# Kernel tuning notes

Hardware: AMD Instinct MI355X
Metric: run time of the kernel (lower is better)

Reference implementation:

```python
import jax, jax.numpy as jnp
import numpy as np

B, D_W, D_C, D_P = 4096, 2048, 1024, 2048
RANK = D_W // 4  # 512, per A_U/A_V shapes (d_w, d_w//4)


def setup_inputs() -> dict:
    key = jax.random.key(0)
    ks = jax.random.split(key, 10)
    return {
        "w_prev": jax.random.normal(ks[0], (B, D_W), jnp.float32),
        "z_t": jax.random.normal(ks[1], (B, D_P), jnp.float32),
        "c_t": jax.random.normal(ks[2], (B, D_C), jnp.float32),
        # params (mirroring flax init: A_diag zeros, A_U/A_V normal(0.01),
        # Dense kernels lecun_normal-ish scale, zero biases)
        "A_diag": jnp.zeros((D_W,), jnp.float32),
        "A_U": 0.01 * jax.random.normal(ks[3], (D_W, RANK), jnp.float32),
        "A_V": 0.01 * jax.random.normal(ks[4], (D_W, RANK), jnp.float32),
        "W_mod": jax.random.normal(ks[5], (D_C, D_W), jnp.float32) / np.sqrt(D_C),
        "b_mod": jnp.zeros((D_W,), jnp.float32),
        "W_B": jax.random.normal(ks[6], (D_C + D_P, D_W), jnp.float32) / np.sqrt(D_C + D_P),
        "b_B": jnp.zeros((D_W,), jnp.float32),
    }


def reference(w_prev, z_t, c_t, A_diag, A_U, A_V, W_mod, b_mod, W_B, b_B):
    # A = diag(tanh(A_diag)*0.9) + A_U @ A_V^T, row-scaled by modulation.
    # Equivalent (same math) without materializing [B, d_w, d_w]:
    #   (A * m[:, :, None]) @ w = m * (a_diag * w + A_U @ (A_V^T @ w))
    a_diag = jnp.tanh(A_diag) * 0.9                              # [d_w]
    modulation = jnp.tanh(c_t @ W_mod + b_mod)                   # [B, d_w]
    Aw = a_diag * w_prev + (w_prev @ A_V) @ A_U.T                # [B, d_w]
    Bt = jnp.concatenate([c_t, z_t], axis=-1) @ W_B + b_B        # [B, d_w]
    return modulation * Aw + Bt
```

## Files before the change

### kernel.cpp

```cpp
#include <hip/hip_runtime.h>


#define DEV __device__ __forceinline__

typedef __bf16 v8bf __attribute__((ext_vector_type(8)));
typedef __bf16 v4bf __attribute__((ext_vector_type(4)));
typedef float  v4f  __attribute__((ext_vector_type(4)));

typedef __attribute__((address_space(1))) const unsigned int* as1_cuint_ptr;
typedef __attribute__((address_space(3))) unsigned int*       as3_uint_ptr;

DEV void async16(const void* g, void* l) {
  __builtin_amdgcn_global_load_lds(
      (as1_cuint_ptr)(unsigned long long)g,
      (as3_uint_ptr)(unsigned long long)l,
      16, 0, 0);
}

DEV float tanh_fast(float x) {
  x = fminf(15.f, fmaxf(-15.f, x));
  float e = __expf(2.f * x);
  return (e - 1.f) / (e + 1.f);
}


__global__ void cvt_all(const float* __restrict__ w, const float* __restrict__ z,
                        const float* __restrict__ c, const float* __restrict__ au,
                        const float* __restrict__ av,
                        __bf16* __restrict__ wb, __bf16* __restrict__ zb,
                        __bf16* __restrict__ cb, __bf16* __restrict__ aub,
                        __bf16* __restrict__ avb) {
  int b = blockIdx.x;
  const float* src; __bf16* dst; int off;
  if (b < 8192)        { src = w;  dst = wb;  off = b; }
  else if (b < 16384)  { src = z;  dst = zb;  off = b - 8192; }
  else if (b < 20480)  { src = c;  dst = cb;  off = b - 16384; }
  else if (b < 21504)  { src = au; dst = aub; off = b - 20480; }
  else                 { src = av; dst = avb; off = b - 21504; }
  size_t i = (size_t)off * 1024 + (size_t)threadIdx.x * 4;
  float4 v = *reinterpret_cast<const float4*>(src + i);
  v4bf o;
  o.x = (__bf16)v.x; o.y = (__bf16)v.y; o.z = (__bf16)v.z; o.w = (__bf16)v.w;
  *reinterpret_cast<v4bf*>(dst + i) = o;
}

__global__ void transpose_both(const float* __restrict__ Wmod,
                               const float* __restrict__ WB,
                               __bf16* __restrict__ Wmodt,
                               __bf16* __restrict__ WBt) {
  __shared__ float t[32][33];
  int b = blockIdx.x;
  const float* src; __bf16* dst; int R;
  if (b < 2048) { src = Wmod; dst = Wmodt; R = 1024; }
  else          { b -= 2048; src = WB; dst = WBt; R = 3072; }
  const int c0 = (b & 63) * 32, r0 = (b >> 6) * 32;
  const int C = 2048;
  const int tx = threadIdx.x & 31, ty = threadIdx.x >> 5;
#pragma unroll
  for (int rr = 0; rr < 32; rr += 8)
    t[ty + rr][tx] = src[(size_t)(r0 + ty + rr) * C + c0 + tx];
  __syncthreads();
#pragma unroll
  for (int rr = 0; rr < 32; rr += 8)
    dst[(size_t)(c0 + ty + rr) * R + r0 + tx] = (__bf16)t[tx][ty + rr];
}

__global__ __launch_bounds__(256, 2) void gemm_mt(
    const __bf16* __restrict__ A0, const __bf16* __restrict__ Bt,
    int N, int K, __bf16* __restrict__ out, const float* __restrict__ A_diag) {
  __shared__ __align__(16) __bf16 As[128 * 32];
  __shared__ __align__(16) __bf16 Bs[128 * 32];

  const int tid = threadIdx.x, lane = tid & 63, wid = tid >> 6;
  const int wm = wid >> 1, wn = wid & 1, l16 = lane & 15, quad = lane >> 4;
  const int m0 = blockIdx.y * 128, n0 = blockIdx.x * 128;
  const int sg_row = lane >> 2;
  const int sk = ((lane & 3) ^ ((lane >> 3) & 3)) * 8;
  const int qs = quad ^ ((l16 >> 1) & 3);

  v4f acc[4][4];
#pragma unroll
  for (int i = 0; i < 4; ++i)
#pragma unroll
    for (int j = 0; j < 4; ++j) { v4f zz = {0,0,0,0}; acc[i][j] = zz; }

  for (int k0 = 0; k0 < K; k0 += 32) {
    __syncthreads();
#pragma unroll
    for (int t = 0; t < 2; ++t) {
      const int chunk = wid * 2 + t;
      const int row = chunk * 16 + sg_row;
      async16((const void*)(A0 + (size_t)(m0 + row) * K + k0 + sk),
              (void*)&As[chunk * 512 + lane * 8]);
      async16((const void*)(Bt + (size_t)(n0 + row) * K + k0 + sk),
              (void*)&Bs[chunk * 512 + lane * 8]);
    }
    __syncthreads();
    const v8bf* Ap = reinterpret_cast<const v8bf*>(As);
    const v8bf* Bp = reinterpret_cast<const v8bf*>(Bs);
    v8bf a[4], b[4];
#pragma unroll
    for (int i = 0; i < 4; ++i) a[i] = Ap[(wm * 64 + i * 16 + l16) * 4 + qs];
#pragma unroll
    for (int j = 0; j < 4; ++j) b[j] = Bp[(wn * 64 + j * 16 + l16) * 4 + qs];
#pragma unroll
    for (int i = 0; i < 4; ++i)
#pragma unroll
      for (int j = 0; j < 4; ++j)
        acc[i][j] = __builtin_amdgcn_mfma_f32_16x16x32_bf16(a[i], b[j],
                                                            acc[i][j], 0, 0, 0);
  }

  const int mBase = m0 + wm * 64 + quad * 4;
  const int nBase = n0 + wn * 64 + l16;
#pragma unroll
  for (int j = 0; j < 4; ++j) {
    const int n = nBase + j * 16;
#pragma unroll
    for (int i = 0; i < 4; ++i)
#pragma unroll
      for (int r = 0; r < 4; ++r) {
        const int m = mBase + i * 16 + r;
        float v = acc[i][j][r];
        if (m == n) v += tanh_fast(A_diag[m]) * 0.9f;
        out[(size_t)m * N + n] = (__bf16)v;
      }
  }
}

__global__ __launch_bounds__(256, 2) void fused_main(
    const __bf16* __restrict__ c, const __bf16* __restrict__ z,
    const __bf16* __restrict__ w, const __bf16* __restrict__ Wmodt,
    const __bf16* __restrict__ Mt, const __bf16* __restrict__ WBt,
    const float* __restrict__ b_mod, const float* __restrict__ b_B,
    float* __restrict__ out) {
  constexpr int DC = 1024, DW = 2048, KB = 3072;
  __shared__ __align__(16) __bf16 As[128 * 32];
  __shared__ __align__(16) __bf16 Bs[128 * 32];

  const int tid = threadIdx.x, lane = tid & 63, wid = tid >> 6;
  const int wm = wid >> 1, wn = wid & 1, l16 = lane & 15, quad = lane >> 4;
  const int m0 = blockIdx.y * 128;
  const int n0 = blockIdx.x * 128;
  const int sg_row = lane >> 2;
  const int sk = ((lane & 3) ^ ((lane >> 3) & 3)) * 8;
  const int qs = quad ^ ((l16 >> 1) & 3);
  const int ldsA  = (wid * 2) * 512 + lane * 8;
  const int ldsA2 = (wid * 2 + 1) * 512 + lane * 8;
  const int rowA  = (wid * 2) * 16 + sg_row;
  const int rowA2 = (wid * 2 + 1) * 16 + sg_row;

  v4f acc[4][4];
#pragma unroll
  for (int i = 0; i < 4; ++i)
#pragma unroll
    for (int j = 0; j < 4; ++j) { v4f zz = {0,0,0,0}; acc[i][j] = zz; }

  auto kstep = [&](const __bf16* gA, size_t lda, const __bf16* gB, size_t ldb,
                   int kA, int kB) {
    __syncthreads();
    async16((const void*)(gA + (size_t)(m0 + rowA) * lda + kA + sk),
            (void*)&As[ldsA]);
    async16((const void*)(gB + (size_t)(n0 + rowA) * ldb + kB + sk),
            (void*)&Bs[ldsA]);
    async16((const void*)(gA + (size_t)(m0 + rowA2) * lda + kA + sk),
            (void*)&As[ldsA2]);
    async16((const void*)(gB + (size_t)(n0 + rowA2) * ldb + kB + sk),
            (void*)&Bs[ldsA2]);
    __syncthreads();
    const v8bf* Ap = reinterpret_cast<const v8bf*>(As);
    const v8bf* Bp = reinterpret_cast<const v8bf*>(Bs);
    v8bf a[4], b[4];
#pragma unroll
    for (int i = 0; i < 4; ++i) a[i] = Ap[(wm * 64 + i * 16 + l16) * 4 + qs];
#pragma unroll
    for (int j = 0; j < 4; ++j) b[j] = Bp[(wn * 64 + j * 16 + l16) * 4 + qs];
#pragma unroll
    for (int i = 0; i < 4; ++i)
#pragma unroll
      for (int j = 0; j < 4; ++j)
        acc[i][j] = __builtin_amdgcn_mfma_f32_16x16x32_bf16(a[i], b[j],
                                                            acc[i][j], 0, 0, 0);
  };

  const int nBase = n0 + wn * 64 + l16;

  for (int k0 = 0; k0 < DC; k0 += 32) kstep(c, DC, Wmodt, DC, k0, k0);

  v4f mod_s[4][4];
#pragma unroll
  for (int j = 0; j < 4; ++j) {
    const float bn = b_mod[nBase + j * 16];
#pragma unroll
    for (int i = 0; i < 4; ++i) {
#pragma unroll
      for (int r = 0; r < 4; ++r)
        mod_s[i][j][r] = tanh_fast(acc[i][j][r] + bn);
      v4f zz = {0,0,0,0};
      acc[i][j] = zz;
    }
  }

  for (int k0 = 0; k0 < DW; k0 += 32) kstep(w, DW, Mt, DW, k0, k0);

#pragma unroll
  for (int i = 0; i < 4; ++i)
#pragma unroll
    for (int j = 0; j < 4; ++j) acc[i][j] *= mod_s[i][j];

  for (int k0 = 0; k0 < DC; k0 += 32) kstep(c, DC, WBt, KB, k0, k0);
  for (int k0 = DC; k0 < KB; k0 += 32) kstep(z, DW, WBt, KB, k0 - DC, k0);

  const int mBase = m0 + wm * 64 + quad * 4;
#pragma unroll
  for (int j = 0; j < 4; ++j) {
    const int n = nBase + j * 16;
    const float bn = b_B[n];
#pragma unroll
    for (int i = 0; i < 4; ++i)
#pragma unroll
      for (int r = 0; r < 4; ++r) {
        const int m = mBase + i * 16 + r;
        out[(size_t)m * DW + n] = acc[i][j][r] + bn;
      }
  }
}


extern "C" void kernel_launch(void* const* d_in, const int* in_sizes, int n_in,
                              void* d_out, int out_size, void* d_ws,
                              size_t ws_size, hipStream_t stream) {
  const float* w_prev = (const float*)d_in[0];
  const float* z_t    = (const float*)d_in[1];
  const float* c_t    = (const float*)d_in[2];
  const float* A_diag = (const float*)d_in[3];
  const float* A_U    = (const float*)d_in[4];
  const float* A_V    = (const float*)d_in[5];
  const float* W_mod  = (const float*)d_in[6];
  const float* b_mod  = (const float*)d_in[7];
  const float* W_B    = (const float*)d_in[8];
  const float* b_B    = (const float*)d_in[9];

  constexpr int Bsz = 4096, DW = 2048, RK = 512;
  const size_t MB = 1ull << 20;
  char* ws = (char*)d_ws;
  __bf16* w_bf  = (__bf16*)(ws + 0);
  __bf16* z_bf  = (__bf16*)(ws + 16 * MB);
  __bf16* c_bf  = (__bf16*)(ws + 32 * MB);
  __bf16* AU_bf = (__bf16*)(ws + 40 * MB);
  __bf16* AV_bf = (__bf16*)(ws + 42 * MB);
  __bf16* Wmodt = (__bf16*)(ws + 44 * MB);
  __bf16* WBt   = (__bf16*)(ws + 48 * MB);
  __bf16* Mt    = (__bf16*)(ws + 60 * MB);

  cvt_all<<<22528, 256, 0, stream>>>(w_prev, z_t, c_t, A_U, A_V,
                                     w_bf, z_bf, c_bf, AU_bf, AV_bf);
  transpose_both<<<2048 + 6144, 256, 0, stream>>>(W_mod, W_B, Wmodt, WBt);

  gemm_mt<<<dim3(DW / 128, DW / 128), 256, 0, stream>>>(AU_bf, AV_bf, DW, RK,
                                                        Mt, A_diag);

  fused_main<<<dim3(DW / 128, Bsz / 128), 256, 0, stream>>>(
      c_bf, z_bf, w_bf, Wmodt, Mt, WBt, b_mod, b_B, (float*)d_out);
}
```

Measured before the change: 314.3 us.

## Shrink fused GEMM tile to 128x64 with higher occupancy; merge prep kernels

The main fused GEMM now uses 128x64 output tiles instead of 128x128, with half the accumulator registers per warp, and raises launch bounds to 4 blocks per CU. This doubles the block count (1024 blocks) for better latency hiding with the single-buffered, synchronous-per-kstep loads. It also merges the conversion and transpose prep kernels into one launch to save a launch gap. The trade-off is lower arithmetic intensity: A tiles get reloaded twice as often, and there are more MFMA-unfriendly syncs per flop.

```diff
diff --git a/kernel.cpp b/kernel.cpp
--- a/kernel.cpp
+++ b/kernel.cpp
@@ -23,33 +23,31 @@
   return (e - 1.f) / (e + 1.f);
 }
 
-
-__global__ void cvt_all(const float* __restrict__ w, const float* __restrict__ z,
-                        const float* __restrict__ c, const float* __restrict__ au,
-                        const float* __restrict__ av,
-                        __bf16* __restrict__ wb, __bf16* __restrict__ zb,
-                        __bf16* __restrict__ cb, __bf16* __restrict__ aub,
-                        __bf16* __restrict__ avb) {
-  int b = blockIdx.x;
-  const float* src; __bf16* dst; int off;
-  if (b < 8192)        { src = w;  dst = wb;  off = b; }
-  else if (b < 16384)  { src = z;  dst = zb;  off = b - 8192; }
-  else if (b < 20480)  { src = c;  dst = cb;  off = b - 16384; }
-  else if (b < 21504)  { src = au; dst = aub; off = b - 20480; }
-  else                 { src = av; dst = avb; off = b - 21504; }
-  size_t i = (size_t)off * 1024 + (size_t)threadIdx.x * 4;
-  float4 v = *reinterpret_cast<const float4*>(src + i);
-  v4bf o;
-  o.x = (__bf16)v.x; o.y = (__bf16)v.y; o.z = (__bf16)v.z; o.w = (__bf16)v.w;
-  *reinterpret_cast<v4bf*>(dst + i) = o;
-}
-
-__global__ void transpose_both(const float* __restrict__ Wmod,
-                               const float* __restrict__ WB,
-                               __bf16* __restrict__ Wmodt,
-                               __bf16* __restrict__ WBt) {
+__global__ void prep(const float* __restrict__ w, const float* __restrict__ z,
+                     const float* __restrict__ c, const float* __restrict__ au,
+                     const float* __restrict__ av,
+                     const float* __restrict__ Wmod, const float* __restrict__ WB,
+                     __bf16* __restrict__ wb, __bf16* __restrict__ zb,
+                     __bf16* __restrict__ cb, __bf16* __restrict__ aub,
+                     __bf16* __restrict__ avb,
+                     __bf16* __restrict__ Wmodt, __bf16* __restrict__ WBt) {
   __shared__ float t[32][33];
   int b = blockIdx.x;
+  if (b < 22528) {
+    const float* src; __bf16* dst; int off;
+    if (b < 8192)        { src = w;  dst = wb;  off = b; }
+    else if (b < 16384)  { src = z;  dst = zb;  off = b - 8192; }
+    else if (b < 20480)  { src = c;  dst = cb;  off = b - 16384; }
+    else if (b < 21504)  { src = au; dst = aub; off = b - 20480; }
+    else                 { src = av; dst = avb; off = b - 21504; }
+    size_t i = (size_t)off * 1024 + (size_t)threadIdx.x * 4;
+    float4 v = *reinterpret_cast<const float4*>(src + i);
+    v4bf o;
+    o.x = (__bf16)v.x; o.y = (__bf16)v.y; o.z = (__bf16)v.z; o.w = (__bf16)v.w;
+    *reinterpret_cast<v4bf*>(dst + i) = o;
+    return;
+  }
+  b -= 22528;
   const float* src; __bf16* dst; int R;
   if (b < 2048) { src = Wmod; dst = Wmodt; R = 1024; }
   else          { b -= 2048; src = WB; dst = WBt; R = 3072; }
@@ -128,7 +126,7 @@
   }
 }
 
-__global__ __launch_bounds__(256, 2) void fused_main(
+__global__ __launch_bounds__(256, 4) void fused_main(
     const __bf16* __restrict__ c, const __bf16* __restrict__ z,
     const __bf16* __restrict__ w, const __bf16* __restrict__ Wmodt,
     const __bf16* __restrict__ Mt, const __bf16* __restrict__ WBt,
@@ -136,60 +134,60 @@
     float* __restrict__ out) {
   constexpr int DC = 1024, DW = 2048, KB = 3072;
   __shared__ __align__(16) __bf16 As[128 * 32];
-  __shared__ __align__(16) __bf16 Bs[128 * 32];
+  __shared__ __align__(16) __bf16 Bs[64 * 32];
 
   const int tid = threadIdx.x, lane = tid & 63, wid = tid >> 6;
   const int wm = wid >> 1, wn = wid & 1, l16 = lane & 15, quad = lane >> 4;
   const int m0 = blockIdx.y * 128;
-  const int n0 = blockIdx.x * 128;
+  const int n0 = blockIdx.x * 64;
   const int sg_row = lane >> 2;
   const int sk = ((lane & 3) ^ ((lane >> 3) & 3)) * 8;
   const int qs = quad ^ ((l16 >> 1) & 3);
-  const int ldsA  = (wid * 2) * 512 + lane * 8;
-  const int ldsA2 = (wid * 2 + 1) * 512 + lane * 8;
-  const int rowA  = (wid * 2) * 16 + sg_row;
-  const int rowA2 = (wid * 2 + 1) * 16 + sg_row;
-
-  v4f acc[4][4];
+  const int rowA0 = wid * 32 + sg_row;
+  const int rowA1 = wid * 32 + 16 + sg_row;
+  const int rowB  = wid * 16 + sg_row;
+  const int ldsA0 = (wid * 2) * 512 + lane * 8;
+  const int ldsA1 = (wid * 2 + 1) * 512 + lane * 8;
+  const int ldsB  = wid * 512 + lane * 8;
+
+  v4f acc[4][2];
 #pragma unroll
   for (int i = 0; i < 4; ++i)
 #pragma unroll
-    for (int j = 0; j < 4; ++j) { v4f zz = {0,0,0,0}; acc[i][j] = zz; }
+    for (int j = 0; j < 2; ++j) { v4f zz = {0,0,0,0}; acc[i][j] = zz; }
 
   auto kstep = [&](const __bf16* gA, size_t lda, const __bf16* gB, size_t ldb,
                    int kA, int kB) {
     __syncthreads();
-    async16((const void*)(gA + (size_t)(m0 + rowA) * lda + kA + sk),
-            (void*)&As[ldsA]);
-    async16((const void*)(gB + (size_t)(n0 + rowA) * ldb + kB + sk),
-            (void*)&Bs[ldsA]);
-    async16((const void*)(gA + (size_t)(m0 + rowA2) * lda + kA + sk),
-            (void*)&As[ldsA2]);
-    async16((const void*)(gB + (size_t)(n0 + rowA2) * ldb + kB + sk),
-            (void*)&Bs[ldsA2]);
+    async16((const void*)(gA + (size_t)(m0 + rowA0) * lda + kA + sk),
+            (void*)&As[ldsA0]);
+    async16((const void*)(gA + (size_t)(m0 + rowA1) * lda + kA + sk),
+            (void*)&As[ldsA1]);
+    async16((const void*)(gB + (size_t)(n0 + rowB) * ldb + kB + sk),
+            (void*)&Bs[ldsB]);
     __syncthreads();
     const v8bf* Ap = reinterpret_cast<const v8bf*>(As);
     const v8bf* Bp = reinterpret_cast<const v8bf*>(Bs);
-    v8bf a[4], b[4];
+    v8bf a[4], b[2];
 #pragma unroll
     for (int i = 0; i < 4; ++i) a[i] = Ap[(wm * 64 + i * 16 + l16) * 4 + qs];
 #pragma unroll
-    for (int j = 0; j < 4; ++j) b[j] = Bp[(wn * 64 + j * 16 + l16) * 4 + qs];
-#pragma unroll
-    for (int i = 0; i < 4; ++i)
-#pragma unroll
-      for (int j = 0; j < 4; ++j)
+    for (int j = 0; j < 2; ++j) b[j] = Bp[(wn * 32 + j * 16 + l16) * 4 + qs];
+#pragma unroll
+    for (int i = 0; i < 4; ++i)
+#pragma unroll
+      for (int j = 0; j < 2; ++j)
         acc[i][j] = __builtin_amdgcn_mfma_f32_16x16x32_bf16(a[i], b[j],
                                                             acc[i][j], 0, 0, 0);
   };
 
-  const int nBase = n0 + wn * 64 + l16;
+  const int nBase = n0 + wn * 32 + l16;
 
   for (int k0 = 0; k0 < DC; k0 += 32) kstep(c, DC, Wmodt, DC, k0, k0);
 
-  v4f mod_s[4][4];
-#pragma unroll
-  for (int j = 0; j < 4; ++j) {
+  v4f mod_s[4][2];
+#pragma unroll
+  for (int j = 0; j < 2; ++j) {
     const float bn = b_mod[nBase + j * 16];
 #pragma unroll
     for (int i = 0; i < 4; ++i) {
@@ -206,14 +204,14 @@
 #pragma unroll
   for (int i = 0; i < 4; ++i)
 #pragma unroll
-    for (int j = 0; j < 4; ++j) acc[i][j] *= mod_s[i][j];
+    for (int j = 0; j < 2; ++j) acc[i][j] *= mod_s[i][j];
 
   for (int k0 = 0; k0 < DC; k0 += 32) kstep(c, DC, WBt, KB, k0, k0);
   for (int k0 = DC; k0 < KB; k0 += 32) kstep(z, DW, WBt, KB, k0 - DC, k0);
 
   const int mBase = m0 + wm * 64 + quad * 4;
 #pragma unroll
-  for (int j = 0; j < 4; ++j) {
+  for (int j = 0; j < 2; ++j) {
     const int n = nBase + j * 16;
     const float bn = b_B[n];
 #pragma unroll
@@ -253,13 +251,12 @@
   __bf16* WBt   = (__bf16*)(ws + 48 * MB);
   __bf16* Mt    = (__bf16*)(ws + 60 * MB);
 
-  cvt_all<<<22528, 256, 0, stream>>>(w_prev, z_t, c_t, A_U, A_V,
-                                     w_bf, z_bf, c_bf, AU_bf, AV_bf);
-  transpose_both<<<2048 + 6144, 256, 0, stream>>>(W_mod, W_B, Wmodt, WBt);
+  prep<<<30720, 256, 0, stream>>>(w_prev, z_t, c_t, A_U, A_V, W_mod, W_B,
+                                  w_bf, z_bf, c_bf, AU_bf, AV_bf, Wmodt, WBt);
 
   gemm_mt<<<dim3(DW / 128, DW / 128), 256, 0, stream>>>(AU_bf, AV_bf, DW, RK,
                                                         Mt, A_diag);
 
-  fused_main<<<dim3(DW / 128, Bsz / 128), 256, 0, stream>>>(
+  fused_main<<<dim3(DW / 64, Bsz / 128), 256, 0, stream>>>(
       c_bf, z_bf, w_bf, Wmodt, Mt, WBt, b_mod, b_B, (float*)d_out);
 }
```

Measured after the change: 335.5 us. +6.7%, slower.

## Double K-tile depth in fused GEMM and merge prep kernels into one launch

Applied to the files above, without the earlier changes.

The fused main kernel now stages 64-wide K slices per iteration instead of 32, with a new 8-way XOR swizzle for the LDS layout. Each slice is consumed as two MFMA passes, which halves the number of barrier pairs per K loop. The conversion and transpose kernels are merged into a single launch to save one kernel launch gap. LDS use per block doubles, but it stays small, so two blocks per CU still fit.

```diff
diff --git a/kernel.cpp b/kernel.cpp
--- a/kernel.cpp
+++ b/kernel.cpp
@@ -23,33 +23,31 @@
   return (e - 1.f) / (e + 1.f);
 }
 
-
-__global__ void cvt_all(const float* __restrict__ w, const float* __restrict__ z,
-                        const float* __restrict__ c, const float* __restrict__ au,
-                        const float* __restrict__ av,
-                        __bf16* __restrict__ wb, __bf16* __restrict__ zb,
-                        __bf16* __restrict__ cb, __bf16* __restrict__ aub,
-                        __bf16* __restrict__ avb) {
-  int b = blockIdx.x;
-  const float* src; __bf16* dst; int off;
-  if (b < 8192)        { src = w;  dst = wb;  off = b; }
-  else if (b < 16384)  { src = z;  dst = zb;  off = b - 8192; }
-  else if (b < 20480)  { src = c;  dst = cb;  off = b - 16384; }
-  else if (b < 21504)  { src = au; dst = aub; off = b - 20480; }
-  else                 { src = av; dst = avb; off = b - 21504; }
-  size_t i = (size_t)off * 1024 + (size_t)threadIdx.x * 4;
-  float4 v = *reinterpret_cast<const float4*>(src + i);
-  v4bf o;
-  o.x = (__bf16)v.x; o.y = (__bf16)v.y; o.z = (__bf16)v.z; o.w = (__bf16)v.w;
-  *reinterpret_cast<v4bf*>(dst + i) = o;
-}
-
-__global__ void transpose_both(const float* __restrict__ Wmod,
-                               const float* __restrict__ WB,
-                               __bf16* __restrict__ Wmodt,
-                               __bf16* __restrict__ WBt) {
+__global__ void prep(const float* __restrict__ w, const float* __restrict__ z,
+                     const float* __restrict__ c, const float* __restrict__ au,
+                     const float* __restrict__ av,
+                     const float* __restrict__ Wmod, const float* __restrict__ WB,
+                     __bf16* __restrict__ wb, __bf16* __restrict__ zb,
+                     __bf16* __restrict__ cb, __bf16* __restrict__ aub,
+                     __bf16* __restrict__ avb,
+                     __bf16* __restrict__ Wmodt, __bf16* __restrict__ WBt) {
   __shared__ float t[32][33];
   int b = blockIdx.x;
+  if (b < 22528) {
+    const float* src; __bf16* dst; int off;
+    if (b < 8192)        { src = w;  dst = wb;  off = b; }
+    else if (b < 16384)  { src = z;  dst = zb;  off = b - 8192; }
+    else if (b < 20480)  { src = c;  dst = cb;  off = b - 16384; }
+    else if (b < 21504)  { src = au; dst = aub; off = b - 20480; }
+    else                 { src = av; dst = avb; off = b - 21504; }
+    size_t i = (size_t)off * 1024 + (size_t)threadIdx.x * 4;
+    float4 v = *reinterpret_cast<const float4*>(src + i);
+    v4bf o;
+    o.x = (__bf16)v.x; o.y = (__bf16)v.y; o.z = (__bf16)v.z; o.w = (__bf16)v.w;
+    *reinterpret_cast<v4bf*>(dst + i) = o;
+    return;
+  }
+  b -= 22528;
   const float* src; __bf16* dst; int R;
   if (b < 2048) { src = Wmod; dst = Wmodt; R = 1024; }
   else          { b -= 2048; src = WB; dst = WBt; R = 3072; }
@@ -135,20 +133,17 @@
     const float* __restrict__ b_mod, const float* __restrict__ b_B,
     float* __restrict__ out) {
   constexpr int DC = 1024, DW = 2048, KB = 3072;
-  __shared__ __align__(16) __bf16 As[128 * 32];
-  __shared__ __align__(16) __bf16 Bs[128 * 32];
+  __shared__ __align__(16) __bf16 As[128 * 64];
+  __shared__ __align__(16) __bf16 Bs[128 * 64];
 
   const int tid = threadIdx.x, lane = tid & 63, wid = tid >> 6;
   const int wm = wid >> 1, wn = wid & 1, l16 = lane & 15, quad = lane >> 4;
   const int m0 = blockIdx.y * 128;
   const int n0 = blockIdx.x * 128;
-  const int sg_row = lane >> 2;
-  const int sk = ((lane & 3) ^ ((lane >> 3) & 3)) * 8;
-  const int qs = quad ^ ((l16 >> 1) & 3);
-  const int ldsA  = (wid * 2) * 512 + lane * 8;
-  const int ldsA2 = (wid * 2 + 1) * 512 + lane * 8;
-  const int rowA  = (wid * 2) * 16 + sg_row;
-  const int rowA2 = (wid * 2 + 1) * 16 + sg_row;
+  const int lrow = lane >> 3;
+  const int skel = ((lane & 7) ^ (lrow & 7)) * 8;
+  const int qs0 = (quad) ^ (l16 & 7);
+  const int qs1 = (4 + quad) ^ (l16 & 7);
 
   v4f acc[4][4];
 #pragma unroll
@@ -159,22 +154,32 @@
   auto kstep = [&](const __bf16* gA, size_t lda, const __bf16* gB, size_t ldb,
                    int kA, int kB) {
     __syncthreads();
-    async16((const void*)(gA + (size_t)(m0 + rowA) * lda + kA + sk),
-            (void*)&As[ldsA]);
-    async16((const void*)(gB + (size_t)(n0 + rowA) * ldb + kB + sk),
-            (void*)&Bs[ldsA]);
-    async16((const void*)(gA + (size_t)(m0 + rowA2) * lda + kA + sk),
-            (void*)&As[ldsA2]);
-    async16((const void*)(gB + (size_t)(n0 + rowA2) * ldb + kB + sk),
-            (void*)&Bs[ldsA2]);
+#pragma unroll
+    for (int t = 0; t < 4; ++t) {
+      const int row = wid * 32 + t * 8 + lrow;
+      async16((const void*)(gA + (size_t)(m0 + row) * lda + kA + skel),
+              (void*)&As[row * 64 + (lane & 7) * 8]);
+      async16((const void*)(gB + (size_t)(n0 + row) * ldb + kB + skel),
+              (void*)&Bs[row * 64 + (lane & 7) * 8]);
+    }
     __syncthreads();
     const v8bf* Ap = reinterpret_cast<const v8bf*>(As);
     const v8bf* Bp = reinterpret_cast<const v8bf*>(Bs);
     v8bf a[4], b[4];
 #pragma unroll
-    for (int i = 0; i < 4; ++i) a[i] = Ap[(wm * 64 + i * 16 + l16) * 4 + qs];
-#pragma unroll
-    for (int j = 0; j < 4; ++j) b[j] = Bp[(wn * 64 + j * 16 + l16) * 4 + qs];
+    for (int i = 0; i < 4; ++i) a[i] = Ap[(wm * 64 + i * 16 + l16) * 8 + qs0];
+#pragma unroll
+    for (int j = 0; j < 4; ++j) b[j] = Bp[(wn * 64 + j * 16 + l16) * 8 + qs0];
+#pragma unroll
+    for (int i = 0; i < 4; ++i)
+#pragma unroll
+      for (int j = 0; j < 4; ++j)
+        acc[i][j] = __builtin_amdgcn_mfma_f32_16x16x32_bf16(a[i], b[j],
+                                                            acc[i][j], 0, 0, 0);
+#pragma unroll
+    for (int i = 0; i < 4; ++i) a[i] = Ap[(wm * 64 + i * 16 + l16) * 8 + qs1];
+#pragma unroll
+    for (int j = 0; j < 4; ++j) b[j] = Bp[(wn * 64 + j * 16 + l16) * 8 + qs1];
 #pragma unroll
     for (int i = 0; i < 4; ++i)
 #pragma unroll
@@ -185,7 +190,7 @@
 
   const int nBase = n0 + wn * 64 + l16;
 
-  for (int k0 = 0; k0 < DC; k0 += 32) kstep(c, DC, Wmodt, DC, k0, k0);
+  for (int k0 = 0; k0 < DC; k0 += 64) kstep(c, DC, Wmodt, DC, k0, k0);
 
   v4f mod_s[4][4];
 #pragma unroll
@@ -201,15 +206,15 @@
     }
   }
 
-  for (int k0 = 0; k0 < DW; k0 += 32) kstep(w, DW, Mt, DW, k0, k0);
+  for (int k0 = 0; k0 < DW; k0 += 64) kstep(w, DW, Mt, DW, k0, k0);
 
 #pragma unroll
   for (int i = 0; i < 4; ++i)
 #pragma unroll
     for (int j = 0; j < 4; ++j) acc[i][j] *= mod_s[i][j];
 
-  for (int k0 = 0; k0 < DC; k0 += 32) kstep(c, DC, WBt, KB, k0, k0);
-  for (int k0 = DC; k0 < KB; k0 += 32) kstep(z, DW, WBt, KB, k0 - DC, k0);
+  for (int k0 = 0; k0 < DC; k0 += 64) kstep(c, DC, WBt, KB, k0, k0);
+  for (int k0 = DC; k0 < KB; k0 += 64) kstep(z, DW, WBt, KB, k0 - DC, k0);
 
   const int mBase = m0 + wm * 64 + quad * 4;
 #pragma unroll
@@ -253,9 +258,8 @@
   __bf16* WBt   = (__bf16*)(ws + 48 * MB);
   __bf16* Mt    = (__bf16*)(ws + 60 * MB);
 
-  cvt_all<<<22528, 256, 0, stream>>>(w_prev, z_t, c_t, A_U, A_V,
-                                     w_bf, z_bf, c_bf, AU_bf, AV_bf);
-  transpose_both<<<2048 + 6144, 256, 0, stream>>>(W_mod, W_B, Wmodt, WBt);
+  prep<<<30720, 256, 0, stream>>>(w_prev, z_t, c_t, A_U, A_V, W_mod, W_B,
+                                  w_bf, z_bf, c_bf, AU_bf, AV_bf, Wmodt, WBt);
 
   gemm_mt<<<dim3(DW / 128, DW / 128), 256, 0, stream>>>(AU_bf, AV_bf, DW, RK,
                                                         Mt, A_diag);
```

Result: faster. 289.1 us (-8.0%).
